# Kernel tuning notes

Hardware: AMD Instinct MI355X
Metric: run time of the kernel (lower is better)

## Reference

```python
import jax, jax.numpy as jnp
import numpy as np
from jax import lax

B, T, I, H, L, O = 256, 1024, 64, 128, 2, 1


def setup_inputs() -> dict:
    key = jax.random.key(0)
    ks = jax.random.split(key, 4 * L + 3)
    s = 1.0 / np.sqrt(H)  # PyTorch LSTM init scale
    inp = {"x": jax.random.normal(ks[0], (B, T, I), dtype=jnp.float32)}
    for l in range(L):
        in_dim = I if l == 0 else H
        inp[f"W_ih_{l}"] = jax.random.uniform(ks[1 + 4 * l], (4 * H, in_dim), minval=-s, maxval=s)
        inp[f"W_hh_{l}"] = jax.random.uniform(ks[2 + 4 * l], (4 * H, H), minval=-s, maxval=s)
        inp[f"b_ih_{l}"] = jax.random.uniform(ks[3 + 4 * l], (4 * H,), minval=-s, maxval=s)
        inp[f"b_hh_{l}"] = jax.random.uniform(ks[4 + 4 * l], (4 * H,), minval=-s, maxval=s)
    inp["W_lin"] = jax.random.uniform(ks[-2], (O, H), minval=-s, maxval=s)
    inp["b_lin"] = jax.random.uniform(ks[-1], (O,), minval=-s, maxval=s)
    return inp


def _lstm_layer(x, W_ih, W_hh, b_ih, b_hh):
    # x: [B, T, in] -> hidden states [B, T, H]; PyTorch gate order i, f, g, o
    b = b_ih + b_hh
    # precompute input projections for all timesteps (one big GEMM)
    x_proj = jnp.einsum('bti,gi->btg', x, W_ih) + b  # [B, T, 4H]

    def step(carry, xp_t):
        h, c = carry
        gates = xp_t + h @ W_hh.T  # [B, 4H]
        i, f, g, o = jnp.split(gates, 4, axis=-1)
        c = jax.nn.sigmoid(f) * c + jax.nn.sigmoid(i) * jnp.tanh(g)
        h = jax.nn.sigmoid(o) * jnp.tanh(c)
        return (h, c), h

    h0 = jnp.zeros((x.shape[0], W_hh.shape[1]), x.dtype)
    (_, _), hs = lax.scan(step, (h0, h0), jnp.swapaxes(x_proj, 0, 1))
    return jnp.swapaxes(hs, 0, 1)  # [B, T, H]


def reference(x, W_ih_0, W_hh_0, b_ih_0, b_hh_0, W_ih_1, W_hh_1, b_ih_1, b_hh_1, W_lin, b_lin):
    h = _lstm_layer(x, W_ih_0, W_hh_0, b_ih_0, b_hh_0)
    h = _lstm_layer(h, W_ih_1, W_hh_1, b_ih_1, b_hh_1)
    return h[:, -1] @ W_lin.T + b_lin  # [B, O]
```

## Files before the change

kernel.cpp:

```cpp
#include <hip/hip_runtime.h>


typedef __attribute__((ext_vector_type(4))) float f32x4;
typedef _Float16 f16x8 __attribute__((ext_vector_type(8)));

#define NB   256
#define TSEQ 1024
#define II   64
#define HH   128
#define G4   512
#define TC   16
#define NCH  (TSEQ/TC)
#define SCL  0.0009765625f
#define SCLI 1024.f

#define F_WHH0  0
#define F_WHH1  8192
#define F_WIH1  16384
#define F_WIH0  24576
#define F_TOTAL 28672

#define KEEP4I(v) asm volatile("" : "+v"((v).x), "+v"((v).y), "+v"((v).z), "+v"((v).w))

__device__ __forceinline__ float tanh_f(float x){
    float ax = fabsf(x);
    float e  = __expf(2.f*ax);
    float t  = 1.f - 2.f*__builtin_amdgcn_rcpf(e + 1.f);
    return copysignf(t, x);
}
__device__ __forceinline__ f32x4 mfma16(int4 a, f16x8 b, f32x4 c){
    return __builtin_amdgcn_mfma_f32_16x16x32_f16(
        __builtin_bit_cast(f16x8, a), b, c, 0, 0, 0);
}
__device__ __forceinline__ f16x8 ldb(const _Float16* p){
    return __builtin_bit_cast(f16x8, *(const int4*)p);
}

__global__ void pack_w(const float* __restrict__ Wih0, const float* __restrict__ Whh0,
                       const float* __restrict__ Wih1, const float* __restrict__ Whh1,
                       int4* __restrict__ ws)
{
    int fid = blockIdx.x * 256 + threadIdx.x;
    if (fid >= F_TOTAL) return;
    const float* src; int nks; int rb;
    if (fid < F_WHH1)      { src = Whh0; nks = 4; rb = fid; }
    else if (fid < F_WIH1) { src = Whh1; nks = 4; rb = fid - F_WHH1; }
    else if (fid < F_WIH0) { src = Wih1; nks = 4; rb = fid - F_WIH1; }
    else                   { src = Wih0; nks = 2; rb = fid - F_WIH0; }
    int lane = rb & 63;
    int rem  = rb >> 6;
    int s    = rem % nks;
    int t    = (rem / nks) & 3;
    int w    = rem / (nks * 4);
    int row  = t * 128 + w * 16 + (lane & 15);
    int K    = nks * 32;
    int k0   = s * 32 + (lane >> 4) * 8;
    const float* p = src + (size_t)row * K + k0;
    unsigned short us[8];
    #pragma unroll
    for (int j = 0; j < 8; ++j)
        us[j] = __builtin_bit_cast(unsigned short, (_Float16)p[j]);
    int4 o;
    o.x = (int)((unsigned)us[0] | ((unsigned)us[1] << 16));
    o.y = (int)((unsigned)us[2] | ((unsigned)us[3] << 16));
    o.z = (int)((unsigned)us[4] | ((unsigned)us[5] << 16));
    o.w = (int)((unsigned)us[6] | ((unsigned)us[7] << 16));
    ws[fid] = o;
}

template<int LAYER>
__device__ __forceinline__ void serial16(
    int w, int lane, int lk, int lm,
    const int4* __restrict__ ws,
    float (&xp)[TC][G4],
    _Float16 (&hist_hi)[TC+1][136], _Float16 (&hist_lo)[TC+1][136],
    _Float16 (&h1_hi)[2][HH], _Float16 (&h1_lo)[2][HH], float* h1f,
    float& c)
{
    const int F = LAYER ? F_WHH1 : F_WHH0;
    int4 Ahi[4][4];
    #pragma unroll
    for (int t4 = 0; t4 < 4; ++t4)
        #pragma unroll
        for (int s = 0; s < 4; ++s)
            Ahi[t4][s] = ws[F + (((w*4 + t4)*4 + s) << 6) + lane];
    #pragma unroll
    for (int t4 = 0; t4 < 4; ++t4)
        #pragma unroll
        for (int s = 0; s < 4; ++s) KEEP4I(Ahi[t4][s]);

    const int gsel = lm >> 2;
    const int usel = lm & 3;
    const int u    = w*16 + lk*4 + usel;
    const int xpr  = gsel*128 + w*16 + lk*4 + usel;
    const int base = lane & 0x33;
    const bool writer = (gsel == 0);
    const bool is_g   = (gsel == 2);
    const bool odd    = (lane & 1);

    #pragma unroll 1
    for (int t = 0; t < TC; ++t){
        const _Float16* hhp = LAYER ? &h1_hi[t&1][0] : &hist_hi[t][0];
        const _Float16* hlp = LAYER ? &h1_lo[t&1][0] : &hist_lo[t][0];
        const _Float16* bp  = odd ? hlp : hhp;
        float xpv = xp[t][xpr];
        f32x4 acc[4];
        #pragma unroll
        for (int t4 = 0; t4 < 4; ++t4) acc[t4] = (f32x4){0.f,0.f,0.f,0.f};
        #pragma unroll
        for (int s = 0; s < 4; ++s){
            f16x8 bv = ldb(&bp[s*32 + lk*8]);
            #pragma unroll
            for (int t4 = 0; t4 < 4; ++t4) acc[t4] = mfma16(Ahi[t4][s], bv, acc[t4]);
        }
        f32x4 ps;
        {
            f32x4 p01 = (gsel & 1) ? acc[1] : acc[0];
            f32x4 p23 = (gsel & 1) ? acc[3] : acc[2];
            ps = (gsel & 2) ? p23 : p01;
        }
        float own, oth;
        {
            float a01 = (usel & 1) ? ps[1] : ps[0];
            float a23 = (usel & 1) ? ps[3] : ps[2];
            own = (usel & 2) ? a23 : a01;
            float b01 = (usel & 1) ? ps[0] : ps[1];
            float b23 = (usel & 1) ? ps[2] : ps[3];
            oth = (usel & 2) ? b23 : b01;
        }
        float recv = __shfl_xor(oth, 1);
        float pre  = (odd ? (recv + SCL*own) : (own + SCL*recv)) + xpv;
        float z    = tanh_f(is_g ? pre : 0.5f*pre);
        float y    = is_g ? z : 0.5f*z + 0.5f;
        float gi = __shfl(y, base);
        float gf = __shfl(y, base | 4);
        float gg = __shfl(y, base | 8);
        float go = __shfl(y, base | 12);
        c = gf*c + gi*gg;
        float h = go * tanh_f(c);
        _Float16 hf = (_Float16)h;
        _Float16 hl = (_Float16)((h - (float)hf) * SCLI);
        if (writer){
            if (LAYER){
                h1_hi[(t+1)&1][u] = hf; h1_lo[(t+1)&1][u] = hl; h1f[u] = h;
            } else {
                hist_hi[t+1][u] = hf; hist_lo[t+1][u] = hl;
            }
        }
        __syncthreads();
    }
}

__global__ __launch_bounds__(512, 2)
void lstm_mfma(const float* __restrict__ x,
               const float* __restrict__ bih0, const float* __restrict__ bhh0,
               const float* __restrict__ bih1, const float* __restrict__ bhh1,
               const float* __restrict__ Wlin, const float* __restrict__ blin,
               const int4* __restrict__ ws,
               float* __restrict__ out)
{
    const int b    = blockIdx.x;
    const int tid  = threadIdx.x;
    const int lane = tid & 63;
    const int w    = tid >> 6;
    const int lm   = lane & 15;
    const int lk   = lane >> 4;

    __shared__ __align__(16) float    xp[TC][G4];
    __shared__ __align__(16) _Float16 hist_hi[TC+1][136];
    __shared__ __align__(16) _Float16 hist_lo[TC+1][136];
    __shared__ __align__(16) _Float16 xc_hi[TC][72];
    __shared__ __align__(16) _Float16 xc_lo[TC][72];
    __shared__ __align__(16) _Float16 h1_hi[2][HH];
    __shared__ __align__(16) _Float16 h1_lo[2][HH];
    __shared__ __align__(16) float    h1f[HH];
    __shared__ __align__(16) float    bias[2][G4];

    bias[0][tid] = bih0[tid] + bhh0[tid];
    bias[1][tid] = bih1[tid] + bhh1[tid];
    if (tid < HH){ hist_hi[0][tid] = (_Float16)0.f; hist_lo[0][tid] = (_Float16)0.f;
                   h1_hi[0][tid] = (_Float16)0.f; h1_lo[0][tid] = (_Float16)0.f;
                   h1f[tid] = 0.f; }
    float c0 = 0.f, c1 = 0.f;
    const float* xb = x + (size_t)b * TSEQ * II;
    __syncthreads();

    #pragma unroll 1
    for (int ch = 0; ch < NCH; ++ch){
        {
            int i0 = tid, i1 = tid + 512;
            float v0 = xb[(size_t)ch*TC*II + i0];
            float v1 = xb[(size_t)ch*TC*II + i1];
            _Float16 a0 = (_Float16)v0, a1 = (_Float16)v1;
            xc_hi[i0>>6][i0&63] = a0; xc_lo[i0>>6][i0&63] = (_Float16)((v0 - (float)a0)*SCLI);
            xc_hi[i1>>6][i1&63] = a1; xc_lo[i1>>6][i1&63] = (_Float16)((v1 - (float)a1)*SCLI);
        }
        if (ch > 0 && tid < HH){
            hist_hi[0][tid] = hist_hi[TC][tid];
            hist_lo[0][tid] = hist_lo[TC][tid];
        }
        __syncthreads();

        {
            f32x4 acc[4], accL[4];
            #pragma unroll
            for (int t4 = 0; t4 < 4; ++t4){
                acc[t4]  = (f32x4){0.f,0.f,0.f,0.f};
                accL[t4] = (f32x4){0.f,0.f,0.f,0.f};
            }
            #pragma unroll
            for (int s = 0; s < 2; ++s){
                f16x8 bh = ldb(&xc_hi[lm][s*32 + lk*8]);
                f16x8 bl = ldb(&xc_lo[lm][s*32 + lk*8]);
                int4 ah[4];
                #pragma unroll
                for (int t4 = 0; t4 < 4; ++t4)
                    ah[t4] = ws[F_WIH0 + (((w*4 + t4)*2 + s) << 6) + lane];
                #pragma unroll
                for (int t4 = 0; t4 < 4; ++t4) acc[t4]  = mfma16(ah[t4], bh, acc[t4]);
                #pragma unroll
                for (int t4 = 0; t4 < 4; ++t4) accL[t4] = mfma16(ah[t4], bl, accL[t4]);
            }
            #pragma unroll
            for (int t4 = 0; t4 < 4; ++t4){
                int rowb = t4*128 + w*16 + lk*4;
                f32x4 cmb = acc[t4] + accL[t4]*SCL;
                *(f32x4*)&xp[lm][rowb] = cmb + *(const f32x4*)&bias[0][rowb];
            }
        }
        __syncthreads();

        serial16<0>(w, lane, lk, lm, ws, xp, hist_hi, hist_lo,
                    h1_hi, h1_lo, h1f, c0);

        {
            f32x4 acc[4], accL[4];
            #pragma unroll
            for (int t4 = 0; t4 < 4; ++t4){
                acc[t4]  = (f32x4){0.f,0.f,0.f,0.f};
                accL[t4] = (f32x4){0.f,0.f,0.f,0.f};
            }
            #pragma unroll
            for (int s = 0; s < 4; ++s){
                f16x8 bh = ldb(&hist_hi[lm + 1][s*32 + lk*8]);
                f16x8 bl = ldb(&hist_lo[lm + 1][s*32 + lk*8]);
                int4 ah[4];
                #pragma unroll
                for (int t4 = 0; t4 < 4; ++t4)
                    ah[t4] = ws[F_WIH1 + (((w*4 + t4)*4 + s) << 6) + lane];
                #pragma unroll
                for (int t4 = 0; t4 < 4; ++t4) acc[t4]  = mfma16(ah[t4], bh, acc[t4]);
                #pragma unroll
                for (int t4 = 0; t4 < 4; ++t4) accL[t4] = mfma16(ah[t4], bl, accL[t4]);
                if (s == 1) __builtin_amdgcn_sched_barrier(0);
            }
            #pragma unroll
            for (int t4 = 0; t4 < 4; ++t4){
                int rowb = t4*128 + w*16 + lk*4;
                f32x4 cmb = acc[t4] + accL[t4]*SCL;
                *(f32x4*)&xp[lm][rowb] = cmb + *(const f32x4*)&bias[1][rowb];
            }
        }
        __syncthreads();

        serial16<1>(w, lane, lk, lm, ws, xp, hist_hi, hist_lo,
                    h1_hi, h1_lo, h1f, c1);
    }

    if (tid < 64){
        float s = h1f[tid]*Wlin[tid] + h1f[tid+64]*Wlin[tid+64];
        #pragma unroll
        for (int off = 32; off; off >>= 1) s += __shfl_down(s, off);
        if (tid == 0) out[b] = s + blin[0];
    }
}

extern "C" void kernel_launch(void* const* d_in, const int* in_sizes, int n_in,
                              void* d_out, int out_size, void* d_ws, size_t ws_size,
                              hipStream_t stream)
{
    const float* x    = (const float*)d_in[0];
    const float* Wih0 = (const float*)d_in[1];
    const float* Whh0 = (const float*)d_in[2];
    const float* bih0 = (const float*)d_in[3];
    const float* bhh0 = (const float*)d_in[4];
    const float* Wih1 = (const float*)d_in[5];
    const float* Whh1 = (const float*)d_in[6];
    const float* bih1 = (const float*)d_in[7];
    const float* bhh1 = (const float*)d_in[8];
    const float* Wlin = (const float*)d_in[9];
    const float* blin = (const float*)d_in[10];
    int4* ws = (int4*)d_ws;

    hipLaunchKernelGGL(pack_w, dim3(F_TOTAL/256), dim3(256), 0, stream,
                       Wih0, Whh0, Wih1, Whh1, ws);
    hipLaunchKernelGGL(lstm_mfma, dim3(NB), dim3(512), 0, stream,
                       x, bih0, bhh0, bih1, bhh1, Wlin, blin, ws, (float*)d_out);
}
```

Baseline: 1.550 ms.

## Wavefront-pipeline both LSTM layers in one timestep loop with layer-1 weights in LDS

```diff
diff --git a/kernel.cpp b/kernel.cpp
--- a/kernel.cpp
+++ b/kernel.cpp
@@ -9,7 +9,7 @@
 #define II   64
 #define HH   128
 #define G4   512
-#define TC   16
+#define TC   8
 #define NCH  (TSEQ/TC)
 #define SCL  0.0009765625f
 #define SCLI 1024.f
@@ -68,89 +68,6 @@
     ws[fid] = o;
 }
 
-template<int LAYER>
-__device__ __forceinline__ void serial16(
-    int w, int lane, int lk, int lm,
-    const int4* __restrict__ ws,
-    float (&xp)[TC][G4],
-    _Float16 (&hist_hi)[TC+1][136], _Float16 (&hist_lo)[TC+1][136],
-    _Float16 (&h1_hi)[2][HH], _Float16 (&h1_lo)[2][HH], float* h1f,
-    float& c)
-{
-    const int F = LAYER ? F_WHH1 : F_WHH0;
-    int4 Ahi[4][4];
-    #pragma unroll
-    for (int t4 = 0; t4 < 4; ++t4)
-        #pragma unroll
-        for (int s = 0; s < 4; ++s)
-            Ahi[t4][s] = ws[F + (((w*4 + t4)*4 + s) << 6) + lane];
-    #pragma unroll
-    for (int t4 = 0; t4 < 4; ++t4)
-        #pragma unroll
-        for (int s = 0; s < 4; ++s) KEEP4I(Ahi[t4][s]);
-
-    const int gsel = lm >> 2;
-    const int usel = lm & 3;
-    const int u    = w*16 + lk*4 + usel;
-    const int xpr  = gsel*128 + w*16 + lk*4 + usel;
-    const int base = lane & 0x33;
-    const bool writer = (gsel == 0);
-    const bool is_g   = (gsel == 2);
-    const bool odd    = (lane & 1);
-
-    #pragma unroll 1
-    for (int t = 0; t < TC; ++t){
-        const _Float16* hhp = LAYER ? &h1_hi[t&1][0] : &hist_hi[t][0];
-        const _Float16* hlp = LAYER ? &h1_lo[t&1][0] : &hist_lo[t][0];
-        const _Float16* bp  = odd ? hlp : hhp;
-        float xpv = xp[t][xpr];
-        f32x4 acc[4];
-        #pragma unroll
-        for (int t4 = 0; t4 < 4; ++t4) acc[t4] = (f32x4){0.f,0.f,0.f,0.f};
-        #pragma unroll
-        for (int s = 0; s < 4; ++s){
-            f16x8 bv = ldb(&bp[s*32 + lk*8]);
-            #pragma unroll
-            for (int t4 = 0; t4 < 4; ++t4) acc[t4] = mfma16(Ahi[t4][s], bv, acc[t4]);
-        }
-        f32x4 ps;
-        {
-            f32x4 p01 = (gsel & 1) ? acc[1] : acc[0];
-            f32x4 p23 = (gsel & 1) ? acc[3] : acc[2];
-            ps = (gsel & 2) ? p23 : p01;
-        }
-        float own, oth;
-        {
-            float a01 = (usel & 1) ? ps[1] : ps[0];
-            float a23 = (usel & 1) ? ps[3] : ps[2];
-            own = (usel & 2) ? a23 : a01;
-            float b01 = (usel & 1) ? ps[0] : ps[1];
-            float b23 = (usel & 1) ? ps[2] : ps[3];
-            oth = (usel & 2) ? b23 : b01;
-        }
-        float recv = __shfl_xor(oth, 1);
-        float pre  = (odd ? (recv + SCL*own) : (own + SCL*recv)) + xpv;
-        float z    = tanh_f(is_g ? pre : 0.5f*pre);
-        float y    = is_g ? z : 0.5f*z + 0.5f;
-        float gi = __shfl(y, base);
-        float gf = __shfl(y, base | 4);
-        float gg = __shfl(y, base | 8);
-        float go = __shfl(y, base | 12);
-        c = gf*c + gi*gg;
-        float h = go * tanh_f(c);
-        _Float16 hf = (_Float16)h;
-        _Float16 hl = (_Float16)((h - (float)hf) * SCLI);
-        if (writer){
-            if (LAYER){
-                h1_hi[(t+1)&1][u] = hf; h1_lo[(t+1)&1][u] = hl; h1f[u] = h;
-            } else {
-                hist_hi[t+1][u] = hf; hist_lo[t+1][u] = hl;
-            }
-        }
-        __syncthreads();
-    }
-}
-
 __global__ __launch_bounds__(512, 2)
 void lstm_mfma(const float* __restrict__ x,
                const float* __restrict__ bih0, const float* __restrict__ bhh0,
@@ -166,74 +83,79 @@
     const int lm   = lane & 15;
     const int lk   = lane >> 4;
 
-    __shared__ __align__(16) float    xp[TC][G4];
-    __shared__ __align__(16) _Float16 hist_hi[TC+1][136];
-    __shared__ __align__(16) _Float16 hist_lo[TC+1][136];
-    __shared__ __align__(16) _Float16 xc_hi[TC][72];
-    __shared__ __align__(16) _Float16 xc_lo[TC][72];
+    __shared__ __align__(16) int4     Wl1[8][15][64];
+    __shared__ __align__(16) float    xp0[TC][G4];
+    __shared__ __align__(16) float    xp1[TC][G4];
+    __shared__ __align__(16) _Float16 h0_hi[TC+1][HH];
+    __shared__ __align__(16) _Float16 h0_lo[TC+1][HH];
     __shared__ __align__(16) _Float16 h1_hi[2][HH];
     __shared__ __align__(16) _Float16 h1_lo[2][HH];
-    __shared__ __align__(16) float    h1f[HH];
-    __shared__ __align__(16) float    bias[2][G4];
-
-    bias[0][tid] = bih0[tid] + bhh0[tid];
-    bias[1][tid] = bih1[tid] + bhh1[tid];
-    if (tid < HH){ hist_hi[0][tid] = (_Float16)0.f; hist_lo[0][tid] = (_Float16)0.f;
-                   h1_hi[0][tid] = (_Float16)0.f; h1_lo[0][tid] = (_Float16)0.f;
-                   h1f[tid] = 0.f; }
+
+    const int  gsel = lm >> 2;
+    const int  usel = lm & 3;
+    const int  u    = w*16 + lk*4 + usel;
+    const int  xpr  = gsel*128 + w*16 + lk*4 + usel;
+    const int  base = lane & 0x33;
+    const bool writer = (gsel == 0);
+    const bool is_g   = (gsel == 2);
+    const bool odd    = (lane & 1);
+
+    if (tid < HH){
+        h0_hi[0][tid] = (_Float16)0.f; h0_lo[0][tid] = (_Float16)0.f;
+        h1_hi[0][tid] = (_Float16)0.f; h1_lo[0][tid] = (_Float16)0.f;
+    }
+    #pragma unroll
+    for (int f = 0; f < 15; ++f){
+        int t4s = f + 1;
+        Wl1[w][f][lane] =
+            ws[F_WHH1 + (((w*4 + (t4s>>2))*4 + (t4s&3)) << 6) + lane];
+    }
     float c0 = 0.f, c1 = 0.f;
     const float* xb = x + (size_t)b * TSEQ * II;
     __syncthreads();
 
     #pragma unroll 1
-    for (int ch = 0; ch < NCH; ++ch){
-        {
-            int i0 = tid, i1 = tid + 512;
-            float v0 = xb[(size_t)ch*TC*II + i0];
-            float v1 = xb[(size_t)ch*TC*II + i1];
-            _Float16 a0 = (_Float16)v0, a1 = (_Float16)v1;
-            xc_hi[i0>>6][i0&63] = a0; xc_lo[i0>>6][i0&63] = (_Float16)((v0 - (float)a0)*SCLI);
-            xc_hi[i1>>6][i1&63] = a1; xc_lo[i1>>6][i1&63] = (_Float16)((v1 - (float)a1)*SCLI);
-        }
-        if (ch > 0 && tid < HH){
-            hist_hi[0][tid] = hist_hi[TC][tid];
-            hist_lo[0][tid] = hist_lo[TC][tid];
-        }
-        __syncthreads();
-
-        {
+    for (int ch = 0; ch <= NCH; ++ch){
+        const bool l0 = (ch < NCH);
+        const bool l1 = (ch > 0);
+
+        if (l1){
             f32x4 acc[4], accL[4];
             #pragma unroll
             for (int t4 = 0; t4 < 4; ++t4){
                 acc[t4]  = (f32x4){0.f,0.f,0.f,0.f};
                 accL[t4] = (f32x4){0.f,0.f,0.f,0.f};
             }
-            #pragma unroll
-            for (int s = 0; s < 2; ++s){
-                f16x8 bh = ldb(&xc_hi[lm][s*32 + lk*8]);
-                f16x8 bl = ldb(&xc_lo[lm][s*32 + lk*8]);
+            int hr = (lm < 8 ? lm : 7) + 1;
+            #pragma unroll
+            for (int s = 0; s < 4; ++s){
+                f16x8 bh = ldb(&h0_hi[hr][s*32 + lk*8]);
+                f16x8 bl = ldb(&h0_lo[hr][s*32 + lk*8]);
                 int4 ah[4];
                 #pragma unroll
                 for (int t4 = 0; t4 < 4; ++t4)
-                    ah[t4] = ws[F_WIH0 + (((w*4 + t4)*2 + s) << 6) + lane];
+                    ah[t4] = ws[F_WIH1 + (((w*4 + t4)*4 + s) << 6) + lane];
                 #pragma unroll
                 for (int t4 = 0; t4 < 4; ++t4) acc[t4]  = mfma16(ah[t4], bh, acc[t4]);
                 #pragma unroll
                 for (int t4 = 0; t4 < 4; ++t4) accL[t4] = mfma16(ah[t4], bl, accL[t4]);
             }
-            #pragma unroll
-            for (int t4 = 0; t4 < 4; ++t4){
-                int rowb = t4*128 + w*16 + lk*4;
-                f32x4 cmb = acc[t4] + accL[t4]*SCL;
-                *(f32x4*)&xp[lm][rowb] = cmb + *(const f32x4*)&bias[0][rowb];
-            }
-        }
-        __syncthreads();
-
-        serial16<0>(w, lane, lk, lm, ws, xp, hist_hi, hist_lo,
-                    h1_hi, h1_lo, h1f, c0);
-
-        {
+            if (lm < 8){
+                #pragma unroll
+                for (int t4 = 0; t4 < 4; ++t4){
+                    int rowb = t4*128 + w*16 + lk*4;
+                    f32x4 bs = *(const f32x4*)(bih1 + rowb) + *(const f32x4*)(bhh1 + rowb);
+                    *(f32x4*)&xp1[lm][rowb] = acc[t4] + accL[t4]*SCL + bs;
+                }
+            }
+        }
+        if (l0 && ch > 0 && tid < HH){
+            h0_hi[0][tid] = h0_hi[TC][tid];
+            h0_lo[0][tid] = h0_lo[TC][tid];
+        }
+        if (l0){
+            int trow = ch*TC + lm; if (trow > TSEQ-1) trow = TSEQ-1;
+            const float* xr = xb + (size_t)trow * II;
             f32x4 acc[4], accL[4];
             #pragma unroll
             for (int t4 = 0; t4 < 4; ++t4){
@@ -241,34 +163,151 @@
                 accL[t4] = (f32x4){0.f,0.f,0.f,0.f};
             }
             #pragma unroll
-            for (int s = 0; s < 4; ++s){
-                f16x8 bh = ldb(&hist_hi[lm + 1][s*32 + lk*8]);
-                f16x8 bl = ldb(&hist_lo[lm + 1][s*32 + lk*8]);
+            for (int s = 0; s < 2; ++s){
+                float4 va = *(const float4*)(xr + s*32 + lk*8);
+                float4 vb = *(const float4*)(xr + s*32 + lk*8 + 4);
+                float vv[8] = {va.x,va.y,va.z,va.w,vb.x,vb.y,vb.z,vb.w};
+                f16x8 bh, bl;
+                #pragma unroll
+                for (int j = 0; j < 8; ++j){
+                    _Float16 hi = (_Float16)vv[j];
+                    bh[j] = hi;
+                    bl[j] = (_Float16)((vv[j] - (float)hi)*SCLI);
+                }
                 int4 ah[4];
                 #pragma unroll
                 for (int t4 = 0; t4 < 4; ++t4)
-                    ah[t4] = ws[F_WIH1 + (((w*4 + t4)*4 + s) << 6) + lane];
+                    ah[t4] = ws[F_WIH0 + (((w*4 + t4)*2 + s) << 6) + lane];
                 #pragma unroll
                 for (int t4 = 0; t4 < 4; ++t4) acc[t4]  = mfma16(ah[t4], bh, acc[t4]);
                 #pragma unroll
                 for (int t4 = 0; t4 < 4; ++t4) accL[t4] = mfma16(ah[t4], bl, accL[t4]);
-                if (s == 1) __builtin_amdgcn_sched_barrier(0);
-            }
-            #pragma unroll
-            for (int t4 = 0; t4 < 4; ++t4){
-                int rowb = t4*128 + w*16 + lk*4;
-                f32x4 cmb = acc[t4] + accL[t4]*SCL;
-                *(f32x4*)&xp[lm][rowb] = cmb + *(const f32x4*)&bias[1][rowb];
+            }
+            if (lm < 8){
+                #pragma unroll
+                for (int t4 = 0; t4 < 4; ++t4){
+                    int rowb = t4*128 + w*16 + lk*4;
+                    f32x4 bs = *(const f32x4*)(bih0 + rowb) + *(const f32x4*)(bhh0 + rowb);
+                    *(f32x4*)&xp0[lm][rowb] = acc[t4] + accL[t4]*SCL + bs;
+                }
             }
         }
         __syncthreads();
 
-        serial16<1>(w, lane, lk, lm, ws, xp, hist_hi, hist_lo,
-                    h1_hi, h1_lo, h1f, c1);
+        int4 Ahi0[4][4], Al1_00;
+        if (l0 || l1){
+            #pragma unroll
+            for (int t4 = 0; t4 < 4; ++t4)
+                #pragma unroll
+                for (int s = 0; s < 4; ++s)
+                    Ahi0[t4][s] = ws[F_WHH0 + (((w*4 + t4)*4 + s) << 6) + lane];
+            Al1_00 = ws[F_WHH1 + (((w*4 + 0)*4 + 0) << 6) + lane];
+            #pragma unroll
+            for (int t4 = 0; t4 < 4; ++t4)
+                #pragma unroll
+                for (int s = 0; s < 4; ++s) KEEP4I(Ahi0[t4][s]);
+            KEEP4I(Al1_00);
+        }
+
+        #pragma unroll 1
+        for (int t = 0; t < TC; ++t){
+            if (l0){
+                const _Float16* bp = odd ? &h0_lo[t][0] : &h0_hi[t][0];
+                float xpv = xp0[t][xpr];
+                f32x4 acc[4];
+                #pragma unroll
+                for (int t4 = 0; t4 < 4; ++t4) acc[t4] = (f32x4){0.f,0.f,0.f,0.f};
+                #pragma unroll
+                for (int s = 0; s < 4; ++s){
+                    f16x8 bv = ldb(&bp[s*32 + lk*8]);
+                    #pragma unroll
+                    for (int t4 = 0; t4 < 4; ++t4) acc[t4] = mfma16(Ahi0[t4][s], bv, acc[t4]);
+                }
+                f32x4 ps;
+                {
+                    f32x4 p01 = (gsel & 1) ? acc[1] : acc[0];
+                    f32x4 p23 = (gsel & 1) ? acc[3] : acc[2];
+                    ps = (gsel & 2) ? p23 : p01;
+                }
+                float own, oth;
+                {
+                    float a01 = (usel & 1) ? ps[1] : ps[0];
+                    float a23 = (usel & 1) ? ps[3] : ps[2];
+                    own = (usel & 2) ? a23 : a01;
+                    float b01 = (usel & 1) ? ps[0] : ps[1];
+                    float b23 = (usel & 1) ? ps[2] : ps[3];
+                    oth = (usel & 2) ? b23 : b01;
+                }
+                float recv = __shfl_xor(oth, 1);
+                float pre  = (odd ? (recv + SCL*own) : (own + SCL*recv)) + xpv;
+                float z    = tanh_f(is_g ? pre : 0.5f*pre);
+                float y    = is_g ? z : 0.5f*z + 0.5f;
+                float gi = __shfl(y, base);
+                float gf = __shfl(y, base | 4);
+                float gg = __shfl(y, base | 8);
+                float go = __shfl(y, base | 12);
+                c0 = gf*c0 + gi*gg;
+                float h = go * tanh_f(c0);
+                _Float16 hf = (_Float16)h;
+                _Float16 hl = (_Float16)((h - (float)hf) * SCLI);
+                if (writer){ h0_hi[t+1][u] = hf; h0_lo[t+1][u] = hl; }
+            }
+            if (l1){
+                const _Float16* bp1 = odd ? &h1_lo[t&1][0] : &h1_hi[t&1][0];
+                float xpv1 = xp1[t][xpr];
+                f32x4 acc[4];
+                #pragma unroll
+                for (int t4 = 0; t4 < 4; ++t4) acc[t4] = (f32x4){0.f,0.f,0.f,0.f};
+                #pragma unroll
+                for (int s = 0; s < 4; ++s){
+                    f16x8 bv = ldb(&bp1[s*32 + lk*8]);
+                    int4 f0 = (s == 0) ? Al1_00 : Wl1[w][s-1][lane];
+                    int4 f1 = Wl1[w][s+3][lane];
+                    int4 f2 = Wl1[w][s+7][lane];
+                    int4 f3 = Wl1[w][s+11][lane];
+                    acc[0] = mfma16(f0, bv, acc[0]);
+                    acc[1] = mfma16(f1, bv, acc[1]);
+                    acc[2] = mfma16(f2, bv, acc[2]);
+                    acc[3] = mfma16(f3, bv, acc[3]);
+                    __builtin_amdgcn_sched_barrier(0);
+                }
+                f32x4 ps;
+                {
+                    f32x4 p01 = (gsel & 1) ? acc[1] : acc[0];
+                    f32x4 p23 = (gsel & 1) ? acc[3] : acc[2];
+                    ps = (gsel & 2) ? p23 : p01;
+                }
+                float own, oth;
+                {
+                    float a01 = (usel & 1) ? ps[1] : ps[0];
+                    float a23 = (usel & 1) ? ps[3] : ps[2];
+                    own = (usel & 2) ? a23 : a01;
+                    float b01 = (usel & 1) ? ps[0] : ps[1];
+                    float b23 = (usel & 1) ? ps[2] : ps[3];
+                    oth = (usel & 2) ? b23 : b01;
+                }
+                float recv = __shfl_xor(oth, 1);
+                float pre  = (odd ? (recv + SCL*own) : (own + SCL*recv)) + xpv1;
+                float z    = tanh_f(is_g ? pre : 0.5f*pre);
+                float y    = is_g ? z : 0.5f*z + 0.5f;
+                float gi = __shfl(y, base);
+                float gf = __shfl(y, base | 4);
+                float gg = __shfl(y, base | 8);
+                float go = __shfl(y, base | 12);
+                c1 = gf*c1 + gi*gg;
+                float h = go * tanh_f(c1);
+                _Float16 hf = (_Float16)h;
+                _Float16 hl = (_Float16)((h - (float)hf) * SCLI);
+                if (writer){ h1_hi[(t+1)&1][u] = hf; h1_lo[(t+1)&1][u] = hl; }
+            }
+            __syncthreads();
+        }
     }
 
     if (tid < 64){
-        float s = h1f[tid]*Wlin[tid] + h1f[tid+64]*Wlin[tid+64];
+        float ha = (float)h1_hi[0][tid]    + (float)h1_lo[0][tid]    * SCL;
+        float hb = (float)h1_hi[0][tid+64] + (float)h1_lo[0][tid+64] * SCL;
+        float s = ha*Wlin[tid] + hb*Wlin[tid+64];
         #pragma unroll
         for (int off = 32; off; off >>= 1) s += __shfl_down(s, off);
         if (tid == 0) out[b] = s + blin[0];
```

Result: slower. 1.679 ms (+8.3%).

## Split LSTM layers into producer/consumer blocks pipelined via global flags

Applied to the files above, without the earlier changes.

```diff
diff --git a/kernel.cpp b/kernel.cpp
--- a/kernel.cpp
+++ b/kernel.cpp
@@ -3,16 +3,17 @@
 
 typedef __attribute__((ext_vector_type(4))) float f32x4;
 typedef _Float16 f16x8 __attribute__((ext_vector_type(8)));
-
-#define NB   256
-#define TSEQ 1024
-#define II   64
-#define HH   128
-#define G4   512
-#define TC   16
-#define NCH  (TSEQ/TC)
-#define SCL  0.0009765625f
-#define SCLI 1024.f
+typedef short s16x8 __attribute__((ext_vector_type(8)));
+
+#define NB    256
+#define TSEQ  1024
+#define II    64
+#define HH    128
+#define G4    512
+#define TC    16
+#define NCH   (TSEQ/TC)
+#define SCL   0.0009765625f
+#define SCLI  1024.f
 
 #define F_WHH0  0
 #define F_WHH1  8192
@@ -20,6 +21,11 @@
 #define F_WIH0  24576
 #define F_TOTAL 28672
 
+#define H0G_OFF   458752ULL
+#define H0G_WORDS (256ULL*1024ULL*128ULL)
+#define FLAG_OFF  (H0G_OFF + H0G_WORDS*4ULL)
+#define WS_NEEDED (FLAG_OFF + 1024ULL)
+
 #define KEEP4I(v) asm volatile("" : "+v"((v).x), "+v"((v).y), "+v"((v).z), "+v"((v).w))
 
 __device__ __forceinline__ float tanh_f(float x){
@@ -34,6 +40,19 @@
 }
 __device__ __forceinline__ f16x8 ldb(const _Float16* p){
     return __builtin_bit_cast(f16x8, *(const int4*)p);
+}
+__device__ __forceinline__ void unpack8(int4 v0, int4 v1, f16x8& bh, f16x8& bl){
+    s16x8 hb, lb;
+    hb[0]=(short)v0.x; lb[0]=(short)(((unsigned)v0.x)>>16);
+    hb[1]=(short)v0.y; lb[1]=(short)(((unsigned)v0.y)>>16);
+    hb[2]=(short)v0.z; lb[2]=(short)(((unsigned)v0.z)>>16);
+    hb[3]=(short)v0.w; lb[3]=(short)(((unsigned)v0.w)>>16);
+    hb[4]=(short)v1.x; lb[4]=(short)(((unsigned)v1.x)>>16);
+    hb[5]=(short)v1.y; lb[5]=(short)(((unsigned)v1.y)>>16);
+    hb[6]=(short)v1.z; lb[6]=(short)(((unsigned)v1.z)>>16);
+    hb[7]=(short)v1.w; lb[7]=(short)(((unsigned)v1.w)>>16);
+    bh = __builtin_bit_cast(f16x8, hb);
+    bl = __builtin_bit_cast(f16x8, lb);
 }
 
 __global__ void pack_w(const float* __restrict__ Wih0, const float* __restrict__ Whh0,
@@ -68,210 +87,268 @@
     ws[fid] = o;
 }
 
-template<int LAYER>
-__device__ __forceinline__ void serial16(
-    int w, int lane, int lk, int lm,
-    const int4* __restrict__ ws,
-    float (&xp)[TC][G4],
-    _Float16 (&hist_hi)[TC+1][136], _Float16 (&hist_lo)[TC+1][136],
-    _Float16 (&h1_hi)[2][HH], _Float16 (&h1_lo)[2][HH], float* h1f,
-    float& c)
+struct LaneCtx {
+    int gsel, usel, u, xpr, base;
+    bool writer, is_g, odd;
+    int lk;
+};
+
+template<bool PING>
+__device__ __forceinline__ void serial_steps(
+    const LaneCtx& L, const int4 (&Ahi)[4][4],
+    float (*xp)[G4],
+    _Float16* hh_rd_base, _Float16* hl_rd_base, int rd_stride,
+    _Float16* hh_wr_base, _Float16* hl_wr_base, int wr_stride,
+    float* h1f, float& c)
 {
-    const int F = LAYER ? F_WHH1 : F_WHH0;
-    int4 Ahi[4][4];
-    #pragma unroll
-    for (int t4 = 0; t4 < 4; ++t4)
-        #pragma unroll
-        for (int s = 0; s < 4; ++s)
-            Ahi[t4][s] = ws[F + (((w*4 + t4)*4 + s) << 6) + lane];
-    #pragma unroll
-    for (int t4 = 0; t4 < 4; ++t4)
-        #pragma unroll
-        for (int s = 0; s < 4; ++s) KEEP4I(Ahi[t4][s]);
-
-    const int gsel = lm >> 2;
-    const int usel = lm & 3;
-    const int u    = w*16 + lk*4 + usel;
-    const int xpr  = gsel*128 + w*16 + lk*4 + usel;
-    const int base = lane & 0x33;
-    const bool writer = (gsel == 0);
-    const bool is_g   = (gsel == 2);
-    const bool odd    = (lane & 1);
-
     #pragma unroll 1
     for (int t = 0; t < TC; ++t){
-        const _Float16* hhp = LAYER ? &h1_hi[t&1][0] : &hist_hi[t][0];
-        const _Float16* hlp = LAYER ? &h1_lo[t&1][0] : &hist_lo[t][0];
-        const _Float16* bp  = odd ? hlp : hhp;
-        float xpv = xp[t][xpr];
+        int rs = PING ? (t & 1) : t;
+        int wsl = PING ? ((t+1) & 1) : (t+1);
+        const _Float16* bp = L.odd ? (hl_rd_base + rs*rd_stride)
+                                   : (hh_rd_base + rs*rd_stride);
+        float xpv = xp[t][L.xpr];
         f32x4 acc[4];
         #pragma unroll
         for (int t4 = 0; t4 < 4; ++t4) acc[t4] = (f32x4){0.f,0.f,0.f,0.f};
         #pragma unroll
         for (int s = 0; s < 4; ++s){
-            f16x8 bv = ldb(&bp[s*32 + lk*8]);
+            f16x8 bv = ldb(&bp[s*32 + L.lk*8]);
             #pragma unroll
             for (int t4 = 0; t4 < 4; ++t4) acc[t4] = mfma16(Ahi[t4][s], bv, acc[t4]);
         }
         f32x4 ps;
         {
-            f32x4 p01 = (gsel & 1) ? acc[1] : acc[0];
-            f32x4 p23 = (gsel & 1) ? acc[3] : acc[2];
-            ps = (gsel & 2) ? p23 : p01;
+            f32x4 p01 = (L.gsel & 1) ? acc[1] : acc[0];
+            f32x4 p23 = (L.gsel & 1) ? acc[3] : acc[2];
+            ps = (L.gsel & 2) ? p23 : p01;
         }
         float own, oth;
         {
-            float a01 = (usel & 1) ? ps[1] : ps[0];
-            float a23 = (usel & 1) ? ps[3] : ps[2];
-            own = (usel & 2) ? a23 : a01;
-            float b01 = (usel & 1) ? ps[0] : ps[1];
-            float b23 = (usel & 1) ? ps[2] : ps[3];
-            oth = (usel & 2) ? b23 : b01;
+            float a01 = (L.usel & 1) ? ps[1] : ps[0];
+            float a23 = (L.usel & 1) ? ps[3] : ps[2];
+            own = (L.usel & 2) ? a23 : a01;
+            float b01 = (L.usel & 1) ? ps[0] : ps[1];
+            float b23 = (L.usel & 1) ? ps[2] : ps[3];
+            oth = (L.usel & 2) ? b23 : b01;
         }
         float recv = __shfl_xor(oth, 1);
-        float pre  = (odd ? (recv + SCL*own) : (own + SCL*recv)) + xpv;
-        float z    = tanh_f(is_g ? pre : 0.5f*pre);
-        float y    = is_g ? z : 0.5f*z + 0.5f;
-        float gi = __shfl(y, base);
-        float gf = __shfl(y, base | 4);
-        float gg = __shfl(y, base | 8);
-        float go = __shfl(y, base | 12);
+        float pre  = (L.odd ? (recv + SCL*own) : (own + SCL*recv)) + xpv;
+        float z    = tanh_f(L.is_g ? pre : 0.5f*pre);
+        float y    = L.is_g ? z : 0.5f*z + 0.5f;
+        float gi = __shfl(y, L.base);
+        float gf = __shfl(y, L.base | 4);
+        float gg = __shfl(y, L.base | 8);
+        float go = __shfl(y, L.base | 12);
         c = gf*c + gi*gg;
         float h = go * tanh_f(c);
         _Float16 hf = (_Float16)h;
         _Float16 hl = (_Float16)((h - (float)hf) * SCLI);
-        if (writer){
-            if (LAYER){
-                h1_hi[(t+1)&1][u] = hf; h1_lo[(t+1)&1][u] = hl; h1f[u] = h;
-            } else {
-                hist_hi[t+1][u] = hf; hist_lo[t+1][u] = hl;
-            }
+        if (L.writer){
+            (hh_wr_base + wsl*wr_stride)[L.u] = hf;
+            (hl_wr_base + wsl*wr_stride)[L.u] = hl;
+            if (h1f) h1f[L.u] = h;
         }
         __syncthreads();
     }
 }
 
 __global__ __launch_bounds__(512, 2)
-void lstm_mfma(const float* __restrict__ x,
+void lstm_dual(const float* __restrict__ x,
                const float* __restrict__ bih0, const float* __restrict__ bhh0,
                const float* __restrict__ bih1, const float* __restrict__ bhh1,
                const float* __restrict__ Wlin, const float* __restrict__ blin,
                const int4* __restrict__ ws,
+               unsigned* __restrict__ h0g,
+               int* __restrict__ prod,
                float* __restrict__ out)
 {
-    const int b    = blockIdx.x;
     const int tid  = threadIdx.x;
     const int lane = tid & 63;
     const int w    = tid >> 6;
     const int lm   = lane & 15;
     const int lk   = lane >> 4;
 
-    __shared__ __align__(16) float    xp[TC][G4];
-    __shared__ __align__(16) _Float16 hist_hi[TC+1][136];
-    __shared__ __align__(16) _Float16 hist_lo[TC+1][136];
-    __shared__ __align__(16) _Float16 xc_hi[TC][72];
-    __shared__ __align__(16) _Float16 xc_lo[TC][72];
-    __shared__ __align__(16) _Float16 h1_hi[2][HH];
-    __shared__ __align__(16) _Float16 h1_lo[2][HH];
-    __shared__ __align__(16) float    h1f[HH];
-    __shared__ __align__(16) float    bias[2][G4];
-
-    bias[0][tid] = bih0[tid] + bhh0[tid];
-    bias[1][tid] = bih1[tid] + bhh1[tid];
-    if (tid < HH){ hist_hi[0][tid] = (_Float16)0.f; hist_lo[0][tid] = (_Float16)0.f;
-                   h1_hi[0][tid] = (_Float16)0.f; h1_lo[0][tid] = (_Float16)0.f;
-                   h1f[tid] = 0.f; }
-    float c0 = 0.f, c1 = 0.f;
-    const float* xb = x + (size_t)b * TSEQ * II;
-    __syncthreads();
-
-    #pragma unroll 1
-    for (int ch = 0; ch < NCH; ++ch){
-        {
-            int i0 = tid, i1 = tid + 512;
-            float v0 = xb[(size_t)ch*TC*II + i0];
-            float v1 = xb[(size_t)ch*TC*II + i1];
-            _Float16 a0 = (_Float16)v0, a1 = (_Float16)v1;
-            xc_hi[i0>>6][i0&63] = a0; xc_lo[i0>>6][i0&63] = (_Float16)((v0 - (float)a0)*SCLI);
-            xc_hi[i1>>6][i1&63] = a1; xc_lo[i1>>6][i1&63] = (_Float16)((v1 - (float)a1)*SCLI);
-        }
-        if (ch > 0 && tid < HH){
-            hist_hi[0][tid] = hist_hi[TC][tid];
-            hist_lo[0][tid] = hist_lo[TC][tid];
-        }
+    LaneCtx L;
+    L.gsel = lm >> 2;  L.usel = lm & 3;  L.lk = lk;
+    L.u    = w*16 + lk*4 + L.usel;
+    L.xpr  = L.gsel*128 + w*16 + lk*4 + L.usel;
+    L.base = lane & 0x33;
+    L.writer = (L.gsel == 0);
+    L.is_g   = (L.gsel == 2);
+    L.odd    = (lane & 1);
+
+    __shared__ __align__(16) char smem[46624];
+    float (*xp)[G4] = (float(*)[G4])smem;
+
+    if (blockIdx.x < NB) {
+        const int row = blockIdx.x;
+        _Float16 (*h0_hi)[136] = (_Float16(*)[136])(smem + 32768);
+        _Float16 (*h0_lo)[136] = (_Float16(*)[136])(smem + 37392);
+        _Float16 (*xc_hi)[72]  = (_Float16(*)[72]) (smem + 42016);
+        _Float16 (*xc_lo)[72]  = (_Float16(*)[72]) (smem + 44320);
+
+        if (tid < HH){ h0_hi[0][tid] = (_Float16)0.f; h0_lo[0][tid] = (_Float16)0.f; }
+        float c0 = 0.f;
+        const float* xb = x + (size_t)row * TSEQ * II;
         __syncthreads();
 
-        {
-            f32x4 acc[4], accL[4];
-            #pragma unroll
-            for (int t4 = 0; t4 < 4; ++t4){
-                acc[t4]  = (f32x4){0.f,0.f,0.f,0.f};
-                accL[t4] = (f32x4){0.f,0.f,0.f,0.f};
-            }
-            #pragma unroll
-            for (int s = 0; s < 2; ++s){
-                f16x8 bh = ldb(&xc_hi[lm][s*32 + lk*8]);
-                f16x8 bl = ldb(&xc_lo[lm][s*32 + lk*8]);
-                int4 ah[4];
-                #pragma unroll
-                for (int t4 = 0; t4 < 4; ++t4)
-                    ah[t4] = ws[F_WIH0 + (((w*4 + t4)*2 + s) << 6) + lane];
-                #pragma unroll
-                for (int t4 = 0; t4 < 4; ++t4) acc[t4]  = mfma16(ah[t4], bh, acc[t4]);
-                #pragma unroll
-                for (int t4 = 0; t4 < 4; ++t4) accL[t4] = mfma16(ah[t4], bl, accL[t4]);
-            }
-            #pragma unroll
-            for (int t4 = 0; t4 < 4; ++t4){
-                int rowb = t4*128 + w*16 + lk*4;
-                f32x4 cmb = acc[t4] + accL[t4]*SCL;
-                *(f32x4*)&xp[lm][rowb] = cmb + *(const f32x4*)&bias[0][rowb];
-            }
-        }
+        #pragma unroll 1
+        for (int ch = 0; ch < NCH; ++ch){
+            {
+                int i0 = tid, i1 = tid + 512;
+                float v0 = xb[(size_t)ch*TC*II + i0];
+                float v1 = xb[(size_t)ch*TC*II + i1];
+                _Float16 a0 = (_Float16)v0, a1 = (_Float16)v1;
+                xc_hi[i0>>6][i0&63] = a0; xc_lo[i0>>6][i0&63] = (_Float16)((v0-(float)a0)*SCLI);
+                xc_hi[i1>>6][i1&63] = a1; xc_lo[i1>>6][i1&63] = (_Float16)((v1-(float)a1)*SCLI);
+            }
+            if (ch > 0 && tid < HH){
+                h0_hi[0][tid] = h0_hi[TC][tid];
+                h0_lo[0][tid] = h0_lo[TC][tid];
+            }
+            __syncthreads();
+
+            {
+                f32x4 acc[4], accL[4];
+                #pragma unroll
+                for (int t4 = 0; t4 < 4; ++t4){
+                    acc[t4]  = (f32x4){0.f,0.f,0.f,0.f};
+                    accL[t4] = (f32x4){0.f,0.f,0.f,0.f};
+                }
+                #pragma unroll
+                for (int s = 0; s < 2; ++s){
+                    f16x8 bh = ldb(&xc_hi[lm][s*32 + lk*8]);
+                    f16x8 bl = ldb(&xc_lo[lm][s*32 + lk*8]);
+                    int4 ah[4];
+                    #pragma unroll
+                    for (int t4 = 0; t4 < 4; ++t4)
+                        ah[t4] = ws[F_WIH0 + (((w*4 + t4)*2 + s) << 6) + lane];
+                    #pragma unroll
+                    for (int t4 = 0; t4 < 4; ++t4) acc[t4]  = mfma16(ah[t4], bh, acc[t4]);
+                    #pragma unroll
+                    for (int t4 = 0; t4 < 4; ++t4) accL[t4] = mfma16(ah[t4], bl, accL[t4]);
+                }
+                #pragma unroll
+                for (int t4 = 0; t4 < 4; ++t4){
+                    int rowb = t4*128 + w*16 + lk*4;
+                    f32x4 bs = *(const f32x4*)(bih0+rowb) + *(const f32x4*)(bhh0+rowb);
+                    *(f32x4*)&xp[lm][rowb] = acc[t4] + accL[t4]*SCL + bs;
+                }
+            }
+            __syncthreads();
+
+            int4 Ahi[4][4];
+            #pragma unroll
+            for (int t4 = 0; t4 < 4; ++t4)
+                #pragma unroll
+                for (int s = 0; s < 4; ++s)
+                    Ahi[t4][s] = ws[F_WHH0 + (((w*4 + t4)*4 + s) << 6) + lane];
+            #pragma unroll
+            for (int t4 = 0; t4 < 4; ++t4)
+                #pragma unroll
+                for (int s = 0; s < 4; ++s) KEEP4I(Ahi[t4][s]);
+
+            serial_steps<false>(L, Ahi, xp,
+                                &h0_hi[0][0], &h0_lo[0][0], 136,
+                                &h0_hi[0][0], &h0_lo[0][0], 136,
+                                nullptr, c0);
+
+            {
+                size_t gbase = ((size_t)row*TSEQ + (size_t)ch*TC)*HH;
+                #pragma unroll
+                for (int k = 0; k < 4; ++k){
+                    int idx = tid + 512*k;
+                    int t = idx >> 7, u = idx & 127;
+                    unsigned ph = (unsigned)__builtin_bit_cast(unsigned short, h0_hi[t+1][u]);
+                    unsigned pl = (unsigned)__builtin_bit_cast(unsigned short, h0_lo[t+1][u]);
+                    h0g[gbase + idx] = ph | (pl << 16);
+                }
+            }
+            __syncthreads();
+            if (tid == 0)
+                __hip_atomic_store(&prod[row], ch+1, __ATOMIC_RELEASE,
+                                   __HIP_MEMORY_SCOPE_AGENT);
+        }
+    } else {
+        const int row = blockIdx.x - NB;
+        _Float16 (*h1_hi)[HH] = (_Float16(*)[HH])(smem + 32768);
+        _Float16 (*h1_lo)[HH] = (_Float16(*)[HH])(smem + 33280);
+        float*    h1f         = (float*)(smem + 33792);
+
+        if (tid < HH){ h1_hi[0][tid] = (_Float16)0.f; h1_lo[0][tid] = (_Float16)0.f;
+                       h1f[tid] = 0.f; }
+        float c1 = 0.f;
         __syncthreads();
 
-        serial16<0>(w, lane, lk, lm, ws, xp, hist_hi, hist_lo,
-                    h1_hi, h1_lo, h1f, c0);
-
-        {
-            f32x4 acc[4], accL[4];
-            #pragma unroll
-            for (int t4 = 0; t4 < 4; ++t4){
-                acc[t4]  = (f32x4){0.f,0.f,0.f,0.f};
-                accL[t4] = (f32x4){0.f,0.f,0.f,0.f};
-            }
-            #pragma unroll
-            for (int s = 0; s < 4; ++s){
-                f16x8 bh = ldb(&hist_hi[lm + 1][s*32 + lk*8]);
-                f16x8 bl = ldb(&hist_lo[lm + 1][s*32 + lk*8]);
-                int4 ah[4];
-                #pragma unroll
-                for (int t4 = 0; t4 < 4; ++t4)
-                    ah[t4] = ws[F_WIH1 + (((w*4 + t4)*4 + s) << 6) + lane];
-                #pragma unroll
-                for (int t4 = 0; t4 < 4; ++t4) acc[t4]  = mfma16(ah[t4], bh, acc[t4]);
-                #pragma unroll
-                for (int t4 = 0; t4 < 4; ++t4) accL[t4] = mfma16(ah[t4], bl, accL[t4]);
-                if (s == 1) __builtin_amdgcn_sched_barrier(0);
-            }
-            #pragma unroll
-            for (int t4 = 0; t4 < 4; ++t4){
-                int rowb = t4*128 + w*16 + lk*4;
-                f32x4 cmb = acc[t4] + accL[t4]*SCL;
-                *(f32x4*)&xp[lm][rowb] = cmb + *(const f32x4*)&bias[1][rowb];
-            }
-        }
-        __syncthreads();
-
-        serial16<1>(w, lane, lk, lm, ws, xp, hist_hi, hist_lo,
-                    h1_hi, h1_lo, h1f, c1);
-    }
-
-    if (tid < 64){
-        float s = h1f[tid]*Wlin[tid] + h1f[tid+64]*Wlin[tid+64];
-        #pragma unroll
-        for (int off = 32; off; off >>= 1) s += __shfl_down(s, off);
-        if (tid == 0) out[b] = s + blin[0];
+        #pragma unroll 1
+        for (int ch = 0; ch < NCH; ++ch){
+            {
+                int v = __hip_atomic_load(&prod[row], __ATOMIC_RELAXED,
+                                          __HIP_MEMORY_SCOPE_AGENT);
+                while (v < ch+1){
+                    __builtin_amdgcn_s_sleep(8);
+                    v = __hip_atomic_load(&prod[row], __ATOMIC_RELAXED,
+                                          __HIP_MEMORY_SCOPE_AGENT);
+                }
+                (void)__hip_atomic_load(&prod[row], __ATOMIC_ACQUIRE,
+                                        __HIP_MEMORY_SCOPE_AGENT);
+            }
+            {
+                f32x4 acc[4], accL[4];
+                #pragma unroll
+                for (int t4 = 0; t4 < 4; ++t4){
+                    acc[t4]  = (f32x4){0.f,0.f,0.f,0.f};
+                    accL[t4] = (f32x4){0.f,0.f,0.f,0.f};
+                }
+                size_t gbase = ((size_t)row*TSEQ + (size_t)ch*TC + lm)*HH;
+                #pragma unroll
+                for (int s = 0; s < 4; ++s){
+                    const int4* gp = (const int4*)(h0g + gbase + s*32 + lk*8);
+                    int4 v0 = gp[0], v1 = gp[1];
+                    f16x8 bh, bl;
+                    unpack8(v0, v1, bh, bl);
+                    int4 ah[4];
+                    #pragma unroll
+                    for (int t4 = 0; t4 < 4; ++t4)
+                        ah[t4] = ws[F_WIH1 + (((w*4 + t4)*4 + s) << 6) + lane];
+                    #pragma unroll
+                    for (int t4 = 0; t4 < 4; ++t4) acc[t4]  = mfma16(ah[t4], bh, acc[t4]);
+                    #pragma unroll
+                    for (int t4 = 0; t4 < 4; ++t4) accL[t4] = mfma16(ah[t4], bl, accL[t4]);
+                }
+                #pragma unroll
+                for (int t4 = 0; t4 < 4; ++t4){
+                    int rowb = t4*128 + w*16 + lk*4;
+                    f32x4 bs = *(const f32x4*)(bih1+rowb) + *(const f32x4*)(bhh1+rowb);
+                    *(f32x4*)&xp[lm][rowb] = acc[t4] + accL[t4]*SCL + bs;
+                }
+            }
+            __syncthreads();
+
+            int4 Ahi[4][4];
+            #pragma unroll
+            for (int t4 = 0; t4 < 4; ++t4)
+                #pragma unroll
+                for (int s = 0; s < 4; ++s)
+                    Ahi[t4][s] = ws[F_WHH1 + (((w*4 + t4)*4 + s) << 6) + lane];
+            #pragma unroll
+            for (int t4 = 0; t4 < 4; ++t4)
+                #pragma unroll
+                for (int s = 0; s < 4; ++s) KEEP4I(Ahi[t4][s]);
+
+            serial_steps<true>(L, Ahi, xp,
+                               &h1_hi[0][0], &h1_lo[0][0], HH,
+                               &h1_hi[0][0], &h1_lo[0][0], HH,
+                               h1f, c1);
+        }
+
+        if (tid < 64){
+            float s = h1f[tid]*Wlin[tid] + h1f[tid+64]*Wlin[tid+64];
+            #pragma unroll
+            for (int off = 32; off; off >>= 1) s += __shfl_down(s, off);
+            if (tid == 0) out[row] = s + blin[0];
+        }
     }
 }
 
@@ -290,10 +367,18 @@
     const float* bhh1 = (const float*)d_in[8];
     const float* Wlin = (const float*)d_in[9];
     const float* blin = (const float*)d_in[10];
-    int4* ws = (int4*)d_ws;
-
+
+    if (ws_size < WS_NEEDED) return;
+
+    char* wsb = (char*)d_ws;
+    int4*     ws   = (int4*)wsb;
+    unsigned* h0g  = (unsigned*)(wsb + H0G_OFF);
+    int*      prod = (int*)(wsb + FLAG_OFF);
+
+    (void)hipMemsetAsync(prod, 0, 1024, stream);
     hipLaunchKernelGGL(pack_w, dim3(F_TOTAL/256), dim3(256), 0, stream,
                        Wih0, Whh0, Wih1, Whh1, ws);
-    hipLaunchKernelGGL(lstm_mfma, dim3(NB), dim3(512), 0, stream,
-                       x, bih0, bhh0, bih1, bhh1, Wlin, blin, ws, (float*)d_out);
-}
+    hipLaunchKernelGGL(lstm_dual, dim3(2*NB), dim3(512), 0, stream,
+                       x, bih0, bhh0, bih1, bhh1, Wlin, blin,
+                       ws, h0g, prod, (float*)d_out);
+}
```

Result: slower. 1.692 ms (+9.1%).
